# Kernel optimization log

Hardware: AMD Instinct MI355X
Metric: run time of the kernel (lower is better)

Reference implementation:

```python
import jax, jax.numpy as jnp
import numpy as np

B, T, D = 2, 2048, 512
HEADS, DIM_HEAD, MAX_LAG = 8, 64, 5
INNER = HEADS * DIM_HEAD


def setup_inputs() -> dict:
    key = jax.random.key(0)
    k0, k1, k2, k3, k4 = jax.random.split(key, 5)
    x = jax.random.normal(k0, (B, T, D), dtype=jnp.float32)
    # Linear weights stored as (in, out); torch applies x @ W.T with W (out, in).
    Wq = jax.random.normal(k1, (D, INNER), dtype=jnp.float32) * (1.0 / np.sqrt(D))
    Wk = jax.random.normal(k2, (D, INNER), dtype=jnp.float32) * (1.0 / np.sqrt(D))
    Wv = jax.random.normal(k3, (D, INNER), dtype=jnp.float32) * (1.0 / np.sqrt(D))
    Wo = jax.random.normal(k4, (INNER, D), dtype=jnp.float32) * (1.0 / np.sqrt(INNER))
    bo = jnp.zeros((D,), dtype=jnp.float32)
    # Module's init: lag_weights = log(exp(-lags/(max_lag/3))) = -lags/(max_lag/3)
    lags = jnp.arange(MAX_LAG + 1, dtype=jnp.float32)
    lag_weights = jnp.broadcast_to(-(lags / (MAX_LAG / 3.0)), (HEADS, MAX_LAG + 1)).astype(jnp.float32)
    return {"x": x, "Wq": Wq, "Wk": Wk, "Wv": Wv, "Wo": Wo, "bo": bo, "lag_weights": lag_weights}


def reference(x, Wq, Wk, Wv, Wo, bo, lag_weights):
    b, t, _ = x.shape
    h, dh = HEADS, DIM_HEAD
    scale = dh ** -0.5
    # context defaults to x (self-attention)
    q = (x @ Wq).reshape(b, t, h, dh).transpose(0, 2, 1, 3)  # b h t d
    k = (x @ Wk).reshape(b, t, h, dh).transpose(0, 2, 1, 3)
    v = (x @ Wv).reshape(b, t, h, dh).transpose(0, 2, 1, 3)
    sim = jnp.einsum('bhid,bhjd->bhij', q, k) * scale  # b h t t
    # causal mask: keep j <= i
    causal = jnp.tril(jnp.ones((t, t), dtype=bool))
    neg = -jnp.finfo(sim.dtype).max
    sim = jnp.where(causal[None, None], sim, neg)
    # learned additive time-lag bias: lag_adj[h,i,j] = softmax(lag_weights)[h, clamp(i-j,0,MAX_LAG)]
    ti = jnp.arange(t)
    time_lags = jnp.clip(ti[:, None] - ti[None, :], 0, MAX_LAG)  # t t
    lag_probs = jax.nn.softmax(lag_weights, axis=-1)  # h (L+1)
    lag_adj = lag_probs[:, time_lags]  # h t t
    sim = sim + lag_adj[None]
    attn = jax.nn.softmax(sim, axis=-1)
    out = jnp.einsum('bhij,bhjd->bhid', attn, v)
    out = out.transpose(0, 2, 1, 3).reshape(b, t, h * dh)  # b t inner
    return out @ Wo + bo  # dropout is identity at eval
```

## Files before the change

### kernel.cpp

```cpp
#include <hip/hip_runtime.h>
#include <hip/hip_bf16.h>

#define BB 2
#define TT 2048
#define DD 512
#define HH 8
#define DH 64
#define INNER 512
#define MAXLAG 5

typedef __attribute__((ext_vector_type(8))) short short8;
typedef __attribute__((ext_vector_type(4))) float floatx4;
typedef unsigned short ushort_t;

__device__ inline unsigned short f2bf(float f) {
    unsigned u = __float_as_uint(f);
    unsigned r = (u + 0x7FFFu + ((u >> 16) & 1u)) >> 16;
    return (unsigned short)r;
}
__device__ inline float bf2f(unsigned short u) {
    return __uint_as_float(((unsigned)u) << 16);
}

__device__ __forceinline__ void gload16(ushort_t* lds, const ushort_t* g) {
    __builtin_amdgcn_global_load_lds(
        (const __attribute__((address_space(1))) void*)g,
        (__attribute__((address_space(3))) void*)lds, 16, 0, 0);
}

__global__ __launch_bounds__(256)
void cvt_kernel(const float* __restrict__ x,
                const float* __restrict__ wq, const float* __restrict__ wk,
                const float* __restrict__ wv, const float* __restrict__ wo,
                ushort_t* __restrict__ xb,
                ushort_t* __restrict__ wqkvt, ushort_t* __restrict__ wot)
{
    __shared__ float T[32][33];
    const int bid = blockIdx.x;
    if (bid < 1024) {
        int off = (bid * 256 + threadIdx.x) * 8;
        float4 a = *(const float4*)&x[off];
        float4 b = *(const float4*)&x[off + 4];
        ushort_t t[8];
        t[0] = f2bf(a.x); t[1] = f2bf(a.y); t[2] = f2bf(a.z); t[3] = f2bf(a.w);
        t[4] = f2bf(b.x); t[5] = f2bf(b.y); t[6] = f2bf(b.z); t[7] = f2bf(b.w);
        *(uint4*)&xb[off] = *(const uint4*)t;
        return;
    }
    const int r = bid - 1024;
    const int z = r >> 8;
    const int tile = r & 255;
    const float* s = (z == 0) ? wq : (z == 1) ? wk : (z == 2) ? wv : wo;
    ushort_t*    d = (z < 3) ? (wqkvt + (size_t)z * 512 * 512) : wot;
    const int k0 = (tile & 15) * 32;
    const int n0 = (tile >> 4) * 32;
    {
        const int kk = threadIdx.x >> 3;
        const int n4 = (threadIdx.x & 7) * 4;
        float4 v = *(const float4*)&s[(size_t)(k0 + kk) * 512 + n0 + n4];
        T[kk][n4 + 0] = v.x; T[kk][n4 + 1] = v.y;
        T[kk][n4 + 2] = v.z; T[kk][n4 + 3] = v.w;
    }
    __syncthreads();
    {
        const int nn = threadIdx.x >> 3;
        const int k4 = (threadIdx.x & 7) * 4;
        ushort4 o;
        o.x = f2bf(T[k4 + 0][nn]); o.y = f2bf(T[k4 + 1][nn]);
        o.z = f2bf(T[k4 + 2][nn]); o.w = f2bf(T[k4 + 3][nn]);
        *(ushort4*)&d[(size_t)(n0 + nn) * 512 + k0 + k4] = o;
    }
}

#define QM 128
#define QN 64
#define QKS 32

__global__ __launch_bounds__(256)
void gemm_qkv(const ushort_t* __restrict__ A, const ushort_t* __restrict__ Bw,
              ushort_t* __restrict__ q, ushort_t* __restrict__ k,
              ushort_t* __restrict__ vt)
{
    __shared__ ushort_t As[QM * QKS];
    __shared__ ushort_t Bs[QN * QKS];

    const int tid  = threadIdx.x;
    const int wave = tid >> 6;
    const int lane = tid & 63;
    const int quad = lane >> 4;
    const int l15  = lane & 15;
    const int wr   = wave >> 1;
    const int wc   = wave & 1;
    const int bm   = blockIdx.y * QM;
    const int bn   = blockIdx.x * QN;

    const int ga0 = wave * 128 + lane;
    const int ga1 = ga0 + 64;
    const ushort_t* ap0 = &A[(size_t)(bm + (ga0 >> 2)) * DD + (ga0 & 3) * 8];
    const ushort_t* ap1 = &A[(size_t)(bm + (ga1 >> 2)) * DD + (ga1 & 3) * 8];
    const int gb = wave * 64 + lane;
    const ushort_t* bp = &Bw[(size_t)(bn + (gb >> 2)) * DD + (gb & 3) * 8];
    ushort_t* lA0 = &As[(size_t)(wave * 128) * 8];
    ushort_t* lA1 = lA0 + 64 * 8;
    ushort_t* lB  = &Bs[(size_t)(wave * 64) * 8];

    floatx4 acc[4][2];
#pragma unroll
    for (int i = 0; i < 4; ++i)
#pragma unroll
        for (int j = 0; j < 2; ++j) acc[i][j] = (floatx4){0.f, 0.f, 0.f, 0.f};

    for (int k0 = 0; k0 < DD; k0 += QKS) {
        __syncthreads();
        gload16(lA0, ap0 + k0);
        gload16(lA1, ap1 + k0);
        gload16(lB,  bp  + k0);
        __syncthreads();

        short8 af[4], bfr[2];
#pragma unroll
        for (int mt = 0; mt < 4; ++mt)
            af[mt] = *(const short8*)&As[(((wr * 64 + mt * 16 + l15) << 2) + quad) * 8];
#pragma unroll
        for (int nt = 0; nt < 2; ++nt)
            bfr[nt] = *(const short8*)&Bs[(((wc * 32 + nt * 16 + l15) << 2) + quad) * 8];
#pragma unroll
        for (int mt = 0; mt < 4; ++mt)
#pragma unroll
            for (int nt = 0; nt < 2; ++nt)
                acc[mt][nt] = __builtin_amdgcn_mfma_f32_16x16x32_bf16(
                    af[mt], bfr[nt], acc[mt][nt], 0, 0, 0);
    }

    const int z = bn >> 9;
    if (z == 2) {
#pragma unroll
        for (int mt = 0; mt < 4; ++mt) {
            const int m0 = bm + wr * 64 + mt * 16 + quad * 4;
            const int b  = m0 >> 11;
            const int t0 = m0 & 2047;
#pragma unroll
            for (int nt = 0; nt < 2; ++nt) {
                const int n  = bn + wc * 32 + nt * 16 + l15 - 1024;
                const int h  = n >> 6, dd = n & 63;
                ushort4 o;
                o.x = f2bf(acc[mt][nt][0]); o.y = f2bf(acc[mt][nt][1]);
                o.z = f2bf(acc[mt][nt][2]); o.w = f2bf(acc[mt][nt][3]);
                *(ushort4*)&vt[((size_t)((b * 8 + h) * 64 + dd)) * 2048 + t0] = o;
            }
        }
        return;
    }
    ushort_t* O = (z == 0) ? q : k;
    const int nb = bn - z * 512;
#pragma unroll
    for (int mt = 0; mt < 4; ++mt) {
#pragma unroll
        for (int nt = 0; nt < 2; ++nt) {
            const int n = nb + wc * 32 + nt * 16 + l15;
#pragma unroll
            for (int reg = 0; reg < 4; ++reg) {
                const int m = bm + wr * 64 + mt * 16 + quad * 4 + reg;
                O[(size_t)m * 512 + n] = f2bf(acc[mt][nt][reg]);
            }
        }
    }
}

__global__ __launch_bounds__(256)
void gemm_proj(const ushort_t* __restrict__ A, const ushort_t* __restrict__ Bw,
               float* __restrict__ O, const float* __restrict__ bias)
{
    __shared__ ushort_t As[64 * 32];
    __shared__ ushort_t Bs[64 * 32];

    const int tid  = threadIdx.x;
    const int wave = tid >> 6;
    const int lane = tid & 63;
    const int quad = lane >> 4;
    const int l15  = lane & 15;
    const int wr   = wave >> 1;
    const int wc   = wave & 1;
    const int bm   = blockIdx.y * 64;
    const int bn   = blockIdx.x * 64;

    const ushort_t* ap = &A[(size_t)(bm + (tid >> 2)) * INNER + (tid & 3) * 8];
    const ushort_t* bp = &Bw[(size_t)(bn + (tid >> 2)) * INNER + (tid & 3) * 8];
    ushort_t* lA = &As[(size_t)(wave * 64) * 8];
    ushort_t* lB = &Bs[(size_t)(wave * 64) * 8];

    floatx4 acc[2][2];
#pragma unroll
    for (int i = 0; i < 2; ++i)
#pragma unroll
        for (int j = 0; j < 2; ++j) acc[i][j] = (floatx4){0.f, 0.f, 0.f, 0.f};

    for (int k0 = 0; k0 < INNER; k0 += 32) {
        __syncthreads();
        gload16(lA, ap + k0);
        gload16(lB, bp + k0);
        __syncthreads();

        short8 af[2], bfr[2];
#pragma unroll
        for (int mt = 0; mt < 2; ++mt)
            af[mt] = *(const short8*)&As[(((wr * 32 + mt * 16 + l15) << 2) + quad) * 8];
#pragma unroll
        for (int nt = 0; nt < 2; ++nt)
            bfr[nt] = *(const short8*)&Bs[(((wc * 32 + nt * 16 + l15) << 2) + quad) * 8];
#pragma unroll
        for (int mt = 0; mt < 2; ++mt)
#pragma unroll
            for (int nt = 0; nt < 2; ++nt)
                acc[mt][nt] = __builtin_amdgcn_mfma_f32_16x16x32_bf16(
                    af[mt], bfr[nt], acc[mt][nt], 0, 0, 0);
    }

    float bv[2];
#pragma unroll
    for (int nt = 0; nt < 2; ++nt)
        bv[nt] = bias[bn + wc * 32 + nt * 16 + l15];
#pragma unroll
    for (int mt = 0; mt < 2; ++mt) {
#pragma unroll
        for (int nt = 0; nt < 2; ++nt) {
            const int n = bn + wc * 32 + nt * 16 + l15;
#pragma unroll
            for (int reg = 0; reg < 4; ++reg) {
                const int m = bm + wr * 32 + mt * 16 + quad * 4 + reg;
                O[(size_t)m * 512 + n] = acc[mt][nt][reg] + bv[nt];
            }
        }
    }
}

#define PAD 72
#define MFIX 10.0f

__global__ __launch_bounds__(256)
void attn_mfma(const ushort_t* __restrict__ Qg,
               const ushort_t* __restrict__ Kg,
               const ushort_t* __restrict__ Vtg,
               const float* __restrict__ lagw,
               ushort_t* __restrict__ Opart,
               float* __restrict__ Lpart)
{
    __shared__ ushort_t Ks[64 * 8 * 8];
    __shared__ ushort_t Vts[64 * 8 * 8];
    __shared__ ushort_t Pl[4][16][PAD];

    const int tid  = threadIdx.x;
    const int wave = tid >> 6;
    const int lane = tid & 63;
    const int quad = lane >> 4;
    const int l15  = lane & 15;

    const int bh = blockIdx.y;
    const int b  = bh >> 3;
    const int h  = bh & 7;
    const int c  = blockIdx.x;
    const int qt = 31 - (c >> 1);
    const int sp = c & 1;
    const int i0 = qt * 64;
    const int h1 = (qt + 1) >> 1;
    const int lo = sp ? h1 : 0;
    const int hi = sp ? (qt + 1) : h1;

    float lagb[MAXLAG + 1];
    {
        float mx = -1e30f;
#pragma unroll
        for (int l = 0; l <= MAXLAG; ++l) {
            lagb[l] = lagw[h * (MAXLAG + 1) + l];
            mx = fmaxf(mx, lagb[l]);
        }
        float s = 0.f;
#pragma unroll
        for (int l = 0; l <= MAXLAG; ++l) { lagb[l] = __expf(lagb[l] - mx); s += lagb[l]; }
        float inv = 1.f / s;
#pragma unroll
        for (int l = 0; l <= MAXLAG; ++l) lagb[l] = lagb[l] * inv - MFIX;
    }
    const float c1  = 0.125f;
    const float c2f = lagb[MAXLAG];

    short8 qf0, qf1;
    {
        const ushort_t* qbase =
            Qg + ((size_t)(b * TT + i0 + wave * 16 + l15)) * INNER + h * DH;
        qf0 = *(const short8*)(qbase + quad * 8);
        qf1 = *(const short8*)(qbase + 32 + quad * 8);
    }

    floatx4 oacc[4];
    float lsum[4] = {0.f, 0.f, 0.f, 0.f};
#pragma unroll
    for (int cb = 0; cb < 4; ++cb) oacc[cb] = (floatx4){0.f, 0.f, 0.f, 0.f};

    const int ibase = i0 + wave * 16 + quad * 4;

    const int srow = tid >> 3;
    const int sc   = tid & 7;
    const ushort_t* Kp0 = Kg + ((size_t)(b * TT) + srow) * INNER + h * DH + sc * 8;
    const ushort_t* Kp1 = Kp0 + (size_t)32 * INNER;
    const ushort_t* Vp0 = Vtg + ((size_t)(bh * 64 + srow)) * 2048 + sc * 8;
    const ushort_t* Vp1 = Vp0 + (size_t)32 * 2048;
    const int slot = (sc + srow) & 7;
    const int kdst0 = ((srow << 3) + slot) << 3;
    const int kdst1 = (((srow + 32) << 3) + slot) << 3;

    uint4 pk0, pk1, pv0, pv1;
    if (lo < hi) {
        const size_t koff = (size_t)(lo * 64) * INNER;
        pk0 = *(const uint4*)(Kp0 + koff);
        pk1 = *(const uint4*)(Kp1 + koff);
        pv0 = *(const uint4*)(Vp0 + lo * 64);
        pv1 = *(const uint4*)(Vp1 + lo * 64);
    }

    for (int kt = lo; kt < hi; ++kt) {
        __syncthreads();
        *(uint4*)&Ks[kdst0]  = pk0;
        *(uint4*)&Ks[kdst1]  = pk1;
        *(uint4*)&Vts[kdst0] = pv0;
        *(uint4*)&Vts[kdst1] = pv1;
        if (kt + 1 < hi) {
            const size_t koff = (size_t)((kt + 1) * 64) * INNER;
            pk0 = *(const uint4*)(Kp0 + koff);
            pk1 = *(const uint4*)(Kp1 + koff);
            pv0 = *(const uint4*)(Vp0 + (kt + 1) * 64);
            pv1 = *(const uint4*)(Vp1 + (kt + 1) * 64);
        }
        __syncthreads();

        const int j0 = kt * 64;

        floatx4 sacc[4];
#pragma unroll
        for (int cb = 0; cb < 4; ++cb) {
            const int key = cb * 16 + l15;
            short8 kf0 = *(const short8*)&Ks[((key << 3) + ((quad + key) & 7)) << 3];
            short8 kf1 = *(const short8*)&Ks[((key << 3) + ((quad + 4 + key) & 7)) << 3];
            floatx4 zf = (floatx4){0.f, 0.f, 0.f, 0.f};
            zf = __builtin_amdgcn_mfma_f32_16x16x32_bf16(qf0, kf0, zf, 0, 0, 0);
            zf = __builtin_amdgcn_mfma_f32_16x16x32_bf16(qf1, kf1, zf, 0, 0, 0);
            sacc[cb] = zf;
        }

        float p[4][4];
        if (i0 + wave * 16 - (j0 + 63) >= MAXLAG) {
#pragma unroll
            for (int cb = 0; cb < 4; ++cb)
#pragma unroll
                for (int reg = 0; reg < 4; ++reg)
                    p[cb][reg] = __expf(fmaf(sacc[cb][reg], c1, c2f));
        } else {
#pragma unroll
            for (int cb = 0; cb < 4; ++cb) {
                const int j = j0 + cb * 16 + l15;
#pragma unroll
                for (int reg = 0; reg < 4; ++reg) {
                    const int lag = (ibase + reg) - j;
                    float bias = (lag <= 0) ? lagb[0]
                               : (lag == 1) ? lagb[1]
                               : (lag == 2) ? lagb[2]
                               : (lag == 3) ? lagb[3]
                               : (lag == 4) ? lagb[4] : lagb[5];
                    float e = __expf(fmaf(sacc[cb][reg], c1, bias));
                    p[cb][reg] = (lag < 0) ? 0.f : e;
                }
            }
        }
#pragma unroll
        for (int cb = 0; cb < 4; ++cb)
#pragma unroll
            for (int reg = 0; reg < 4; ++reg)
                lsum[reg] += p[cb][reg];

#pragma unroll
        for (int cb = 0; cb < 4; ++cb)
#pragma unroll
            for (int reg = 0; reg < 4; ++reg)
                Pl[wave][quad * 4 + reg][cb * 16 + l15] = f2bf(p[cb][reg]);

        short8 pf0 = *(const short8*)&Pl[wave][l15][quad * 8];
        short8 pf1 = *(const short8*)&Pl[wave][l15][32 + quad * 8];

#pragma unroll
        for (int cb = 0; cb < 4; ++cb) {
            const int dd = cb * 16 + l15;
            short8 vf0 = *(const short8*)&Vts[((dd << 3) + ((quad + dd) & 7)) << 3];
            short8 vf1 = *(const short8*)&Vts[((dd << 3) + ((quad + 4 + dd) & 7)) << 3];
            oacc[cb] = __builtin_amdgcn_mfma_f32_16x16x32_bf16(pf0, vf0, oacc[cb], 0, 0, 0);
            oacc[cb] = __builtin_amdgcn_mfma_f32_16x16x32_bf16(pf1, vf1, oacc[cb], 0, 0, 0);
        }
    }

#pragma unroll
    for (int reg = 0; reg < 4; ++reg) {
        lsum[reg] += __shfl_xor(lsum[reg], 1);
        lsum[reg] += __shfl_xor(lsum[reg], 2);
        lsum[reg] += __shfl_xor(lsum[reg], 4);
        lsum[reg] += __shfl_xor(lsum[reg], 8);
    }

#pragma unroll
    for (int reg = 0; reg < 4; ++reg) {
        const int row = ibase + reg;
        const size_t obase = ((size_t)(sp * 16 + bh) * TT + row) * 64;
#pragma unroll
        for (int cb = 0; cb < 4; ++cb)
            Opart[obase + cb * 16 + l15] = f2bf(oacc[cb][reg]);
        if (l15 == 0)
            Lpart[(size_t)(sp * 16 + bh) * TT + row] = lsum[reg];
    }
}

#define CMB_UNITS (16 * TT * 16)

__global__ __launch_bounds__(256)
void combine_kernel(const ushort_t* __restrict__ Opart,
                    const float* __restrict__ Lpart,
                    ushort_t* __restrict__ ao)
{
    int u = blockIdx.x * 256 + threadIdx.x;
    const int bh  = u >> 15;
    const int rem = u & 32767;
    const int i   = rem >> 4;
    const int d   = (rem & 15) * 4;
    const int b   = bh >> 3;
    const int h   = bh & 7;

    const size_t p0 = ((size_t)bh * TT + i) * 64 + d;
    const size_t p1 = ((size_t)(16 + bh) * TT + i) * 64 + d;
    ushort4 a0 = *(const ushort4*)&Opart[p0];
    ushort4 a1 = *(const ushort4*)&Opart[p1];
    const float l = Lpart[(size_t)bh * TT + i] + Lpart[(size_t)(16 + bh) * TT + i];
    const float inv = 1.f / l;

    ushort4 o;
    o.x = f2bf((bf2f(a0.x) + bf2f(a1.x)) * inv);
    o.y = f2bf((bf2f(a0.y) + bf2f(a1.y)) * inv);
    o.z = f2bf((bf2f(a0.z) + bf2f(a1.z)) * inv);
    o.w = f2bf((bf2f(a0.w) + bf2f(a1.w)) * inv);
    *(ushort4*)&ao[((size_t)(b * TT + i)) * INNER + h * DH + d] = o;
}

extern "C" void kernel_launch(void* const* d_in, const int* in_sizes, int n_in,
                              void* d_out, int out_size, void* d_ws, size_t ws_size,
                              hipStream_t stream)
{
    const float* x  = (const float*)d_in[0];
    const float* Wq = (const float*)d_in[1];
    const float* Wk = (const float*)d_in[2];
    const float* Wv = (const float*)d_in[3];
    const float* Wo = (const float*)d_in[4];
    const float* bo = (const float*)d_in[5];
    const float* lw = (const float*)d_in[6];
    float* out = (float*)d_out;

    const size_t SZ  = (size_t)BB * TT * INNER;
    const size_t NWE = (size_t)DD * INNER;
    ushort_t* xb    = (ushort_t*)d_ws;
    ushort_t* wqkvt = xb + SZ;
    ushort_t* wot   = wqkvt + 3 * NWE;
    ushort_t* q     = wot + NWE;
    ushort_t* k     = q + SZ;
    ushort_t* vt    = k + SZ;
    ushort_t* opart = vt + SZ;
    float*    lpart = (float*)(opart + 2 * SZ);
    ushort_t* ao    = xb;

    cvt_kernel<<<2048, 256, 0, stream>>>(x, Wq, Wk, Wv, Wo, xb, wqkvt, wot);

    dim3 gQKV(3 * INNER / QN, (BB * TT) / QM);
    gemm_qkv<<<gQKV, 256, 0, stream>>>(xb, wqkvt, q, k, vt);

    dim3 gATT(64, BB * HH);
    attn_mfma<<<gATT, 256, 0, stream>>>(q, k, vt, lw, opart, lpart);

    combine_kernel<<<CMB_UNITS / 256, 256, 0, stream>>>(opart, lpart, ao);

    dim3 gPRJ(DD / 64, (BB * TT) / 64);
    gemm_proj<<<gPRJ, 256, 0, stream>>>(ao, wot, out, bo);
}
```

Before: 139.0 us.

## Drop split-K attention and combine kernel; widen GEMM K-tiles to 64

The attention kernel no longer splits each query tile's key range in two. Each block now processes the full causal range and normalizes and writes bf16 output directly, which removes the combine kernel and the partial O/L buffers. Blocks are remapped so the first half of heads runs the longest query tiles first and the second half runs them in reverse, to balance causal work. Separately, the QKV and projection GEMMs load 64-wide K slices per barrier instead of 32, which halves the number of sync rounds. The cost is half as many attention blocks (512 instead of 1024), which lowers parallelism, plus more LDS per GEMM block.

```diff
diff --git a/kernel.cpp b/kernel.cpp
--- a/kernel.cpp
+++ b/kernel.cpp
@@ -74,7 +74,7 @@
 
 #define QM 128
 #define QN 64
-#define QKS 32
+#define QKS 64
 
 __global__ __launch_bounds__(256)
 void gemm_qkv(const ushort_t* __restrict__ A, const ushort_t* __restrict__ Bw,
@@ -94,15 +94,20 @@
     const int bm   = blockIdx.y * QM;
     const int bn   = blockIdx.x * QN;
 
-    const int ga0 = wave * 128 + lane;
-    const int ga1 = ga0 + 64;
-    const ushort_t* ap0 = &A[(size_t)(bm + (ga0 >> 2)) * DD + (ga0 & 3) * 8];
-    const ushort_t* ap1 = &A[(size_t)(bm + (ga1 >> 2)) * DD + (ga1 & 3) * 8];
-    const int gb = wave * 64 + lane;
-    const ushort_t* bp = &Bw[(size_t)(bn + (gb >> 2)) * DD + (gb & 3) * 8];
-    ushort_t* lA0 = &As[(size_t)(wave * 128) * 8];
-    ushort_t* lA1 = lA0 + 64 * 8;
-    ushort_t* lB  = &Bs[(size_t)(wave * 64) * 8];
+    const int ga = wave * 256 + lane;
+    const ushort_t* ap0 = &A[(size_t)(bm + ((ga +   0) >> 3)) * DD + ((ga +   0) & 7) * 8];
+    const ushort_t* ap1 = &A[(size_t)(bm + ((ga +  64) >> 3)) * DD + ((ga +  64) & 7) * 8];
+    const ushort_t* ap2 = &A[(size_t)(bm + ((ga + 128) >> 3)) * DD + ((ga + 128) & 7) * 8];
+    const ushort_t* ap3 = &A[(size_t)(bm + ((ga + 192) >> 3)) * DD + ((ga + 192) & 7) * 8];
+    const int gb = wave * 128 + lane;
+    const ushort_t* bp0 = &Bw[(size_t)(bn + ((gb +  0) >> 3)) * DD + ((gb +  0) & 7) * 8];
+    const ushort_t* bp1 = &Bw[(size_t)(bn + ((gb + 64) >> 3)) * DD + ((gb + 64) & 7) * 8];
+    ushort_t* lA0 = &As[(size_t)(wave * 256 +   0) * 8];
+    ushort_t* lA1 = &As[(size_t)(wave * 256 +  64) * 8];
+    ushort_t* lA2 = &As[(size_t)(wave * 256 + 128) * 8];
+    ushort_t* lA3 = &As[(size_t)(wave * 256 + 192) * 8];
+    ushort_t* lB0 = &Bs[(size_t)(wave * 128 +  0) * 8];
+    ushort_t* lB1 = &Bs[(size_t)(wave * 128 + 64) * 8];
 
     floatx4 acc[4][2];
 #pragma unroll
@@ -114,22 +119,30 @@
         __syncthreads();
         gload16(lA0, ap0 + k0);
         gload16(lA1, ap1 + k0);
-        gload16(lB,  bp  + k0);
-        __syncthreads();
-
-        short8 af[4], bfr[2];
-#pragma unroll
-        for (int mt = 0; mt < 4; ++mt)
-            af[mt] = *(const short8*)&As[(((wr * 64 + mt * 16 + l15) << 2) + quad) * 8];
-#pragma unroll
-        for (int nt = 0; nt < 2; ++nt)
-            bfr[nt] = *(const short8*)&Bs[(((wc * 32 + nt * 16 + l15) << 2) + quad) * 8];
-#pragma unroll
-        for (int mt = 0; mt < 4; ++mt)
+        gload16(lA2, ap2 + k0);
+        gload16(lA3, ap3 + k0);
+        gload16(lB0, bp0 + k0);
+        gload16(lB1, bp1 + k0);
+        __syncthreads();
+
+#pragma unroll
+        for (int kk = 0; kk < 2; ++kk) {
+            short8 af[4], bfr[2];
+#pragma unroll
+            for (int mt = 0; mt < 4; ++mt)
+                af[mt] = *(const short8*)
+                    &As[(((wr * 64 + mt * 16 + l15) << 3) + (kk << 2) + quad) * 8];
 #pragma unroll
             for (int nt = 0; nt < 2; ++nt)
-                acc[mt][nt] = __builtin_amdgcn_mfma_f32_16x16x32_bf16(
-                    af[mt], bfr[nt], acc[mt][nt], 0, 0, 0);
+                bfr[nt] = *(const short8*)
+                    &Bs[(((wc * 32 + nt * 16 + l15) << 3) + (kk << 2) + quad) * 8];
+#pragma unroll
+            for (int mt = 0; mt < 4; ++mt)
+#pragma unroll
+                for (int nt = 0; nt < 2; ++nt)
+                    acc[mt][nt] = __builtin_amdgcn_mfma_f32_16x16x32_bf16(
+                        af[mt], bfr[nt], acc[mt][nt], 0, 0, 0);
+        }
     }
 
     const int z = bn >> 9;
@@ -171,8 +184,8 @@
 void gemm_proj(const ushort_t* __restrict__ A, const ushort_t* __restrict__ Bw,
                float* __restrict__ O, const float* __restrict__ bias)
 {
-    __shared__ ushort_t As[64 * 32];
-    __shared__ ushort_t Bs[64 * 32];
+    __shared__ ushort_t As[64 * 64];
+    __shared__ ushort_t Bs[64 * 64];
 
     const int tid  = threadIdx.x;
     const int wave = tid >> 6;
@@ -184,10 +197,15 @@
     const int bm   = blockIdx.y * 64;
     const int bn   = blockIdx.x * 64;
 
-    const ushort_t* ap = &A[(size_t)(bm + (tid >> 2)) * INNER + (tid & 3) * 8];
-    const ushort_t* bp = &Bw[(size_t)(bn + (tid >> 2)) * INNER + (tid & 3) * 8];
-    ushort_t* lA = &As[(size_t)(wave * 64) * 8];
-    ushort_t* lB = &Bs[(size_t)(wave * 64) * 8];
+    const int g0 = wave * 128 + lane;
+    const ushort_t* ap0 = &A[(size_t)(bm + ((g0 +  0) >> 3)) * INNER + ((g0 +  0) & 7) * 8];
+    const ushort_t* ap1 = &A[(size_t)(bm + ((g0 + 64) >> 3)) * INNER + ((g0 + 64) & 7) * 8];
+    const ushort_t* bp0 = &Bw[(size_t)(bn + ((g0 +  0) >> 3)) * INNER + ((g0 +  0) & 7) * 8];
+    const ushort_t* bp1 = &Bw[(size_t)(bn + ((g0 + 64) >> 3)) * INNER + ((g0 + 64) & 7) * 8];
+    ushort_t* lA0 = &As[(size_t)(wave * 128 +  0) * 8];
+    ushort_t* lA1 = &As[(size_t)(wave * 128 + 64) * 8];
+    ushort_t* lB0 = &Bs[(size_t)(wave * 128 +  0) * 8];
+    ushort_t* lB1 = &Bs[(size_t)(wave * 128 + 64) * 8];
 
     floatx4 acc[2][2];
 #pragma unroll
@@ -195,25 +213,32 @@
 #pragma unroll
         for (int j = 0; j < 2; ++j) acc[i][j] = (floatx4){0.f, 0.f, 0.f, 0.f};
 
-    for (int k0 = 0; k0 < INNER; k0 += 32) {
-        __syncthreads();
-        gload16(lA, ap + k0);
-        gload16(lB, bp + k0);
-        __syncthreads();
-
-        short8 af[2], bfr[2];
-#pragma unroll
-        for (int mt = 0; mt < 2; ++mt)
-            af[mt] = *(const short8*)&As[(((wr * 32 + mt * 16 + l15) << 2) + quad) * 8];
-#pragma unroll
-        for (int nt = 0; nt < 2; ++nt)
-            bfr[nt] = *(const short8*)&Bs[(((wc * 32 + nt * 16 + l15) << 2) + quad) * 8];
-#pragma unroll
-        for (int mt = 0; mt < 2; ++mt)
+    for (int k0 = 0; k0 < INNER; k0 += 64) {
+        __syncthreads();
+        gload16(lA0, ap0 + k0);
+        gload16(lA1, ap1 + k0);
+        gload16(lB0, bp0 + k0);
+        gload16(lB1, bp1 + k0);
+        __syncthreads();
+
+#pragma unroll
+        for (int kk = 0; kk < 2; ++kk) {
+            short8 af[2], bfr[2];
+#pragma unroll
+            for (int mt = 0; mt < 2; ++mt)
+                af[mt] = *(const short8*)
+                    &As[(((wr * 32 + mt * 16 + l15) << 3) + (kk << 2) + quad) * 8];
 #pragma unroll
             for (int nt = 0; nt < 2; ++nt)
-                acc[mt][nt] = __builtin_amdgcn_mfma_f32_16x16x32_bf16(
-                    af[mt], bfr[nt], acc[mt][nt], 0, 0, 0);
+                bfr[nt] = *(const short8*)
+                    &Bs[(((wc * 32 + nt * 16 + l15) << 3) + (kk << 2) + quad) * 8];
+#pragma unroll
+            for (int mt = 0; mt < 2; ++mt)
+#pragma unroll
+                for (int nt = 0; nt < 2; ++nt)
+                    acc[mt][nt] = __builtin_amdgcn_mfma_f32_16x16x32_bf16(
+                        af[mt], bfr[nt], acc[mt][nt], 0, 0, 0);
+        }
     }
 
     float bv[2];
@@ -242,8 +267,7 @@
                const ushort_t* __restrict__ Kg,
                const ushort_t* __restrict__ Vtg,
                const float* __restrict__ lagw,
-               ushort_t* __restrict__ Opart,
-               float* __restrict__ Lpart)
+               ushort_t* __restrict__ ao)
 {
     __shared__ ushort_t Ks[64 * 8 * 8];
     __shared__ ushort_t Vts[64 * 8 * 8];
@@ -255,16 +279,15 @@
     const int quad = lane >> 4;
     const int l15  = lane & 15;
 
-    const int bh = blockIdx.y;
-    const int b  = bh >> 3;
-    const int h  = bh & 7;
-    const int c  = blockIdx.x;
-    const int qt = 31 - (c >> 1);
-    const int sp = c & 1;
-    const int i0 = qt * 64;
-    const int h1 = (qt + 1) >> 1;
-    const int lo = sp ? h1 : 0;
-    const int hi = sp ? (qt + 1) : h1;
+    const int f    = blockIdx.x + 32 * blockIdx.y;
+    const int half = f >> 8;
+    const int r    = f & 255;
+    const int bh   = (half << 3) | (r >> 5);
+    const int qt   = half ? (r & 31) : (31 - (r & 31));
+    const int b    = bh >> 3;
+    const int h    = bh & 7;
+    const int i0   = qt * 64;
+    const int hi   = qt + 1;
 
     float lagb[MAXLAG + 1];
     {
@@ -309,16 +332,12 @@
     const int kdst0 = ((srow << 3) + slot) << 3;
     const int kdst1 = (((srow + 32) << 3) + slot) << 3;
 
-    uint4 pk0, pk1, pv0, pv1;
-    if (lo < hi) {
-        const size_t koff = (size_t)(lo * 64) * INNER;
-        pk0 = *(const uint4*)(Kp0 + koff);
-        pk1 = *(const uint4*)(Kp1 + koff);
-        pv0 = *(const uint4*)(Vp0 + lo * 64);
-        pv1 = *(const uint4*)(Vp1 + lo * 64);
-    }
-
-    for (int kt = lo; kt < hi; ++kt) {
+    uint4 pk0 = *(const uint4*)Kp0;
+    uint4 pk1 = *(const uint4*)Kp1;
+    uint4 pv0 = *(const uint4*)Vp0;
+    uint4 pv1 = *(const uint4*)Vp1;
+
+    for (int kt = 0; kt < hi; ++kt) {
         __syncthreads();
         *(uint4*)&Ks[kdst0]  = pk0;
         *(uint4*)&Ks[kdst1]  = pk1;
@@ -407,43 +426,12 @@
 #pragma unroll
     for (int reg = 0; reg < 4; ++reg) {
         const int row = ibase + reg;
-        const size_t obase = ((size_t)(sp * 16 + bh) * TT + row) * 64;
+        const float inv = 1.f / lsum[reg];
+        ushort_t* dst = &ao[((size_t)(b * TT + row)) * INNER + h * DH];
 #pragma unroll
         for (int cb = 0; cb < 4; ++cb)
-            Opart[obase + cb * 16 + l15] = f2bf(oacc[cb][reg]);
-        if (l15 == 0)
-            Lpart[(size_t)(sp * 16 + bh) * TT + row] = lsum[reg];
-    }
-}
-
-#define CMB_UNITS (16 * TT * 16)
-
-__global__ __launch_bounds__(256)
-void combine_kernel(const ushort_t* __restrict__ Opart,
-                    const float* __restrict__ Lpart,
-                    ushort_t* __restrict__ ao)
-{
-    int u = blockIdx.x * 256 + threadIdx.x;
-    const int bh  = u >> 15;
-    const int rem = u & 32767;
-    const int i   = rem >> 4;
-    const int d   = (rem & 15) * 4;
-    const int b   = bh >> 3;
-    const int h   = bh & 7;
-
-    const size_t p0 = ((size_t)bh * TT + i) * 64 + d;
-    const size_t p1 = ((size_t)(16 + bh) * TT + i) * 64 + d;
-    ushort4 a0 = *(const ushort4*)&Opart[p0];
-    ushort4 a1 = *(const ushort4*)&Opart[p1];
-    const float l = Lpart[(size_t)bh * TT + i] + Lpart[(size_t)(16 + bh) * TT + i];
-    const float inv = 1.f / l;
-
-    ushort4 o;
-    o.x = f2bf((bf2f(a0.x) + bf2f(a1.x)) * inv);
-    o.y = f2bf((bf2f(a0.y) + bf2f(a1.y)) * inv);
-    o.z = f2bf((bf2f(a0.z) + bf2f(a1.z)) * inv);
-    o.w = f2bf((bf2f(a0.w) + bf2f(a1.w)) * inv);
-    *(ushort4*)&ao[((size_t)(b * TT + i)) * INNER + h * DH + d] = o;
+            dst[cb * 16 + l15] = f2bf(oacc[cb][reg] * inv);
+    }
 }
 
 extern "C" void kernel_launch(void* const* d_in, const int* in_sizes, int n_in,
@@ -467,8 +455,6 @@
     ushort_t* q     = wot + NWE;
     ushort_t* k     = q + SZ;
     ushort_t* vt    = k + SZ;
-    ushort_t* opart = vt + SZ;
-    float*    lpart = (float*)(opart + 2 * SZ);
     ushort_t* ao    = xb;
 
     cvt_kernel<<<2048, 256, 0, stream>>>(x, Wq, Wk, Wv, Wo, xb, wqkvt, wot);
@@ -476,10 +462,8 @@
     dim3 gQKV(3 * INNER / QN, (BB * TT) / QM);
     gemm_qkv<<<gQKV, 256, 0, stream>>>(xb, wqkvt, q, k, vt);
 
-    dim3 gATT(64, BB * HH);
-    attn_mfma<<<gATT, 256, 0, stream>>>(q, k, vt, lw, opart, lpart);
-
-    combine_kernel<<<CMB_UNITS / 256, 256, 0, stream>>>(opart, lpart, ao);
+    dim3 gATT(32, BB * HH);
+    attn_mfma<<<gATT, 256, 0, stream>>>(q, k, vt, lw, ao);
 
     dim3 gPRJ(DD / 64, (BB * TT) / 64);
     gemm_proj<<<gPRJ, 256, 0, stream>>>(ao, wot, out, bo);
```

Result: faster. 130.1 us (-6.4%).
